# Kernel tuning notes

Measured on AMD Instinct MI355X. Metric: run time of the kernel, lower is better.

The kernel has to match this reference:

```python
import jax, jax.numpy as jnp
import numpy as np

B, N, C = 4, 2048, 768
H = 12
HD = C // H

def setup_inputs() -> dict:
    key = jax.random.key(0)
    k1, k2, k3, k4, k5 = jax.random.split(key, 5)
    x = jax.random.normal(k1, (B, N, C), dtype=jnp.float32)
    qkv_w = jax.random.normal(k2, (3 * C, C), dtype=jnp.float32) * (1.0 / np.sqrt(C))
    qkv_b = jax.random.normal(k3, (3 * C,), dtype=jnp.float32) * 0.02
    proj_w = jax.random.normal(k4, (C, C), dtype=jnp.float32) * (1.0 / np.sqrt(C))
    proj_b = jax.random.normal(k5, (C,), dtype=jnp.float32) * 0.02
    return {"x": x, "qkv_w": qkv_w, "qkv_b": qkv_b, "proj_w": proj_w, "proj_b": proj_b}

def reference(x, qkv_w, qkv_b, proj_w, proj_b):
    scale = HD ** (-0.5)
    # qkv projection: (B,N,3C)
    qkv = x @ qkv_w.T + qkv_b
    qkv = qkv.reshape(B, N, 3, H, HD).transpose(2, 0, 3, 1, 4)  # (3,B,H,N,HD)
    q, k, v = qkv[0], qkv[1], qkv[2]
    attn = jnp.einsum('bhqd,bhkd->bhqk', q, k) * scale  # (B,H,N,N)
    mask_value = -jnp.finfo(attn.dtype).max
    causal_mask = jnp.triu(jnp.ones((N, N), dtype=bool), k=1)
    attn = jnp.where(causal_mask, mask_value, attn)
    attn = jax.nn.softmax(attn, axis=-1)
    out = jnp.einsum('bhqk,bhkd->bhqd', attn, v)  # (B,H,N,HD)
    out = out.transpose(0, 2, 1, 3).reshape(B, N, C)
    return out @ proj_w.T + proj_b
```

## Files before the change

### kernel.cpp

```cpp
#include <hip/hip_runtime.h>
#include <hip/hip_bf16.h>


typedef __attribute__((ext_vector_type(8))) short bf16x8;
typedef __attribute__((ext_vector_type(4))) float f32x4;
typedef __attribute__((ext_vector_type(16))) float f32x16;

typedef __attribute__((address_space(3))) unsigned int lds_uint;
typedef __attribute__((address_space(1))) const unsigned int gbl_uint;

__device__ __forceinline__ void gload16(const void* g, void* l) {
  __builtin_amdgcn_global_load_lds((gbl_uint*)g, (lds_uint*)l, 16, 0, 0);
}

__device__ __forceinline__ unsigned short f2bf(float f) {
  unsigned u = __float_as_uint(f);
  unsigned rounding = 0x7FFFu + ((u >> 16) & 1u);
  return (unsigned short)((u + rounding) >> 16);
}

__device__ __forceinline__ unsigned cvtpk(float lo, float hi) {
  unsigned r;
  asm("v_cvt_pk_bf16_f32 %0, %1, %2" : "=v"(r) : "v"(lo), "v"(hi));
  return r;
}

__device__ __forceinline__ float exp2a(float x) {
  float r;
  asm("v_exp_f32 %0, %1" : "=v"(r) : "v"(x));
  return r;
}

__global__ void cast_f32_to_bf16(const float* __restrict__ in,
                                 unsigned short* __restrict__ out, int n) {
  int idx = blockIdx.x * blockDim.x + threadIdx.x;
  int stride = gridDim.x * blockDim.x;
  for (int i = idx * 4; i < n; i += stride * 4) {
    float4 v = *reinterpret_cast<const float4*>(in + i);
    ushort4 o;
    o.x = f2bf(v.x); o.y = f2bf(v.y); o.z = f2bf(v.z); o.w = f2bf(v.w);
    *reinterpret_cast<ushort4*>(out + i) = o;
  }
}

template <bool OUT_F32, int BN>
__global__ __launch_bounds__(256) void gemm_bt_kernel(
    const unsigned short* __restrict__ A,
    const unsigned short* __restrict__ Bw,
    const float* __restrict__ bias,
    void* __restrict__ Cout,
    int M, int Ncols, int K, int ldc, int nblk) {
  constexpr int NFRAG = BN / 32;
  __shared__ __align__(16) short As[2][4096];
  __shared__ __align__(16) short Bs[2][BN * 32];

  const int t = threadIdx.x;
  const int lane = t & 63;
  const int wave = t >> 6;
  const int wm = wave >> 1;
  const int wn = wave & 1;

  const int wid = blockIdx.x;
  const int xcd = wid & 7;
  const int idx = wid >> 3;
  const int m0 = (xcd * 8 + idx / nblk) * 128;
  const int n0 = (idx % nblk) * BN;

  const int lrow = lane & 15;
  const int lk = (lane >> 4) * 8;

  const int srow = t >> 2, scol = (t & 3) * 8;
  const unsigned short* gA0 = A + (size_t)(m0 + srow) * K + scol;
  const unsigned short* gA1 = gA0 + (size_t)64 * K;
  const unsigned short* gB0 = Bw + (size_t)(n0 + srow) * K + scol;
  const unsigned short* gB1 = gB0 + (size_t)64 * K;
  const int db0 = wave * 512, db1 = 2048 + wave * 512;

  f32x4 acc[4][NFRAG] = {};
  const int nk = K / 32;

  gload16(gA0, &As[0][db0]); gload16(gA1, &As[0][db1]);
  gload16(gB0, &Bs[0][db0]);
  if (BN == 128) gload16(gB1, &Bs[0][db1]);

  int cur = 0;
  for (int kk = 0; kk < nk; ++kk) {
    __syncthreads();
    if (kk + 1 < nk) {
      const int off = (kk + 1) * 32;
      gload16(gA0 + off, &As[cur ^ 1][db0]); gload16(gA1 + off, &As[cur ^ 1][db1]);
      gload16(gB0 + off, &Bs[cur ^ 1][db0]);
      if (BN == 128) gload16(gB1 + off, &Bs[cur ^ 1][db1]);
    }
    bf16x8 a[4], b[NFRAG];
#pragma unroll
    for (int m = 0; m < 4; ++m)
      a[m] = *reinterpret_cast<const bf16x8*>(&As[cur][(wm * 64 + m * 16 + lrow) * 32 + lk]);
#pragma unroll
    for (int n = 0; n < NFRAG; ++n)
      b[n] = *reinterpret_cast<const bf16x8*>(&Bs[cur][(wn * (BN / 2) + n * 16 + lrow) * 32 + lk]);
#pragma unroll
    for (int m = 0; m < 4; ++m)
#pragma unroll
      for (int n = 0; n < NFRAG; ++n)
        acc[m][n] = __builtin_amdgcn_mfma_f32_16x16x32_bf16(a[m], b[n], acc[m][n], 0, 0, 0);
    cur ^= 1;
  }

  const int orow0 = (lane >> 4) * 4;
  const int ocol = lane & 15;
#pragma unroll
  for (int m = 0; m < 4; ++m) {
#pragma unroll
    for (int n = 0; n < NFRAG; ++n) {
      const int c = n0 + wn * (BN / 2) + n * 16 + ocol;
      const float bv = bias[c];
#pragma unroll
      for (int r = 0; r < 4; ++r) {
        const int rr = m0 + wm * 64 + m * 16 + orow0 + r;
        const float v = acc[m][n][r] + bv;
        if (OUT_F32)
          reinterpret_cast<float*>(Cout)[(size_t)rr * ldc + c] = v;
        else
          reinterpret_cast<unsigned short*>(Cout)[(size_t)rr * ldc + c] = f2bf(v);
      }
    }
  }
}

#define ATT_N 2048
#define ATT_H 12
#define QKV_LD 2304

__global__ __launch_bounds__(256) void transpose_v(
    const unsigned short* __restrict__ qkv, unsigned short* __restrict__ vt) {
  __shared__ __align__(16) short L[128 * 72];
  const int kb = blockIdx.x;
  const int bh = blockIdx.y;
  const int t = threadIdx.x;
  const int b = bh / ATT_H, h = bh % ATT_H;
  const int d0 = (t & 7) * 8;
  const int kl0 = t >> 3;
  const unsigned short* src =
      qkv + (size_t)(b * ATT_N + kb * 128) * QKV_LD + 1536 + h * 64 + d0;
#pragma unroll
  for (int r = 0; r < 4; ++r) {
    const int kl = kl0 + r * 32;
    bf16x8 v = *reinterpret_cast<const bf16x8*>(src + (size_t)kl * QKV_LD);
    *reinterpret_cast<bf16x8*>(&L[kl * 72 + d0]) = v;
  }
  __syncthreads();
  const int d = t >> 2;
  const int c = t & 3;
  unsigned short* dst = vt + (size_t)bh * 64 * ATT_N + (size_t)d * ATT_N + kb * 128;
#pragma unroll
  for (int cc = 0; cc < 4; ++cc) {
    const int kc = cc * 32 + c * 8;
    union { unsigned short s[8]; bf16x8 v; } U;
#pragma unroll
    for (int j = 0; j < 8; ++j) U.s[j] = (unsigned short)L[(kc + j) * 72 + d];
    *reinterpret_cast<bf16x8*>(dst + kc) = U.v;
  }
}

__global__ __launch_bounds__(256) void attn_kernel(
    const unsigned short* __restrict__ qkv,
    const unsigned short* __restrict__ vt,
    unsigned short* __restrict__ out) {
  __shared__ __align__(16) short Ks[2][4096];
  __shared__ __align__(16) short Vs[2][4096];

  const int t = threadIdx.x;
  const int lane = t & 63;
  const int w = t >> 6;
  const int hi = lane >> 5;
  const int l31 = lane & 31;

  const int wid = blockIdx.x;
  const int qb = 15 - (wid / 48);
  const int bh = wid % 48;
  const int b = bh / ATT_H;
  const int h = bh % ATT_H;

  const size_t rowbase = (size_t)b * ATT_N;
  const unsigned short* qptr = qkv + rowbase * QKV_LD + h * 64;
  const unsigned short* kptr = qptr + 768;
  const unsigned short* vtptr = vt + (size_t)bh * 64 * ATT_N;

  const int q0w = qb * 128 + w * 32;
  const int qg = q0w + l31;
  const int nt = (qb + 1) * 2;

  bf16x8 qf[4];
#pragma unroll
  for (int dk = 0; dk < 4; ++dk)
    qf[dk] = *reinterpret_cast<const bf16x8*>(
        qptr + (size_t)(q0w + l31) * QKV_LD + dk * 16 + hi * 8);

  f32x16 O0 = {}, O1 = {};
  float lrun = 0.f;

  int kKr[2], kKc[2];
#pragma unroll
  for (int c = 0; c < 2; ++c) {
    const int i = t + c * 256;
    const int f = i >> 6, ls = i & 63;
    kKr[c] = (f >> 2) * 32 + (ls & 31);
    kKc[c] = (f & 3) * 2 + (ls >> 5);
  }
  const unsigned short* gK0 = kptr + (size_t)kKr[0] * QKV_LD + kKc[0] * 8;
  const unsigned short* gK1 = kptr + (size_t)kKr[1] * QKV_LD + kKc[1] * 8;
  const unsigned short* gV0 = vtptr + (size_t)kKr[0] * ATT_N + kKc[0] * 8;
  const unsigned short* gV1 = vtptr + (size_t)kKr[1] * ATT_N + kKc[1] * 8;
  const int db0 = w * 512, db1 = 2048 + w * 512;

  gload16(gK0, &Ks[0][db0]); gload16(gK1, &Ks[0][db1]);
  gload16(gV0, &Vs[0][db0]); gload16(gV1, &Vs[0][db1]);

  int cur = 0;
  for (int kt = 0; kt < nt; ++kt) {
    const int k0 = kt * 64;
    __syncthreads();
    if (kt + 1 < nt) {
      const size_t advk = (size_t)(k0 + 64) * QKV_LD;
      gload16(gK0 + advk, &Ks[cur ^ 1][db0]); gload16(gK1 + advk, &Ks[cur ^ 1][db1]);
      gload16(gV0 + (k0 + 64), &Vs[cur ^ 1][db0]);
      gload16(gV1 + (k0 + 64), &Vs[cur ^ 1][db1]);
    }

    if (k0 <= q0w + 31) {
      f32x16 S0 = {}, S1 = {};
      __builtin_amdgcn_s_setprio(1);
#pragma unroll
      for (int dk = 0; dk < 4; ++dk) {
        bf16x8 kf = *reinterpret_cast<const bf16x8*>(&Ks[cur][(dk * 64 + lane) * 8]);
        S0 = __builtin_amdgcn_mfma_f32_32x32x16_bf16(kf, qf[dk], S0, 0, 0, 0);
      }
#pragma unroll
      for (int dk = 0; dk < 4; ++dk) {
        bf16x8 kf = *reinterpret_cast<const bf16x8*>(&Ks[cur][((4 + dk) * 64 + lane) * 8]);
        S1 = __builtin_amdgcn_mfma_f32_32x32x16_bf16(kf, qf[dk], S1, 0, 0, 0);
      }
      __builtin_amdgcn_s_setprio(0);

      const float scale2 = 0.18033688f;
      float p0[16], p1[16];
      if (k0 + 63 <= q0w) {
#pragma unroll
        for (int r = 0; r < 16; ++r) {
          p0[r] = exp2a(S0[r] * scale2);
          p1[r] = exp2a(S1[r] * scale2);
        }
      } else {
#pragma unroll
        for (int r = 0; r < 16; ++r) {
          int row = (r & 3) + 8 * (r >> 2) + 4 * hi;
          float e0 = (k0 + row > qg) ? -1e30f : S0[r] * scale2;
          float e1 = (k0 + 32 + row > qg) ? -1e30f : S1[r] * scale2;
          p0[r] = exp2a(e0);
          p1[r] = exp2a(e1);
        }
      }

      float sa = 0.f, sb = 0.f;
#pragma unroll
      for (int r = 0; r < 16; r += 2) { sa += p0[r] + p1[r]; sb += p0[r + 1] + p1[r + 1]; }
      float rsum = sa + sb;
      rsum += __shfl_xor(rsum, 32);
      lrun += rsum;

      bf16x8 Ub[4];
#pragma unroll
      for (int s = 0; s < 2; ++s) {
        unsigned pu[4][2];
#pragma unroll
        for (int m = 0; m < 4; ++m)
#pragma unroll
          for (int c = 0; c < 2; ++c)
            pu[m][c] = s ? cvtpk(p1[4 * m + 2 * c], p1[4 * m + 2 * c + 1])
                         : cvtpk(p0[4 * m + 2 * c], p0[4 * m + 2 * c + 1]);
#pragma unroll
        for (int tt = 0; tt < 2; ++tt) {
          unsigned s0v = hi ? pu[2 * tt][0] : pu[2 * tt + 1][0];
          unsigned s1v = hi ? pu[2 * tt][1] : pu[2 * tt + 1][1];
          unsigned r0 = __shfl_xor(s0v, 32);
          unsigned r1 = __shfl_xor(s1v, 32);
          union { unsigned u[4]; bf16x8 v; } U;
          U.u[0] = hi ? r0 : pu[2 * tt][0];
          U.u[1] = hi ? r1 : pu[2 * tt][1];
          U.u[2] = hi ? pu[2 * tt + 1][0] : r0;
          U.u[3] = hi ? pu[2 * tt + 1][1] : r1;
          Ub[s * 2 + tt] = U.v;
        }
      }

      __builtin_amdgcn_s_setprio(1);
#pragma unroll
      for (int ks = 0; ks < 4; ++ks) {
        bf16x8 vf0 = *reinterpret_cast<const bf16x8*>(&Vs[cur][(ks * 64 + lane) * 8]);
        O0 = __builtin_amdgcn_mfma_f32_32x32x16_bf16(vf0, Ub[ks], O0, 0, 0, 0);
        bf16x8 vf1 = *reinterpret_cast<const bf16x8*>(&Vs[cur][((4 + ks) * 64 + lane) * 8]);
        O1 = __builtin_amdgcn_mfma_f32_32x32x16_bf16(vf1, Ub[ks], O1, 0, 0, 0);
      }
      __builtin_amdgcn_s_setprio(0);
    }
    cur ^= 1;
  }

  const float inv = 1.0f / lrun;
  unsigned short* orow = out + (rowbase + q0w + l31) * 768 + h * 64;
#pragma unroll
  for (int half = 0; half < 2; ++half) {
    const f32x16& O = half ? O1 : O0;
#pragma unroll
    for (int m = 0; m < 4; ++m) {
      uint2 o2;
      o2.x = cvtpk(O[4 * m + 0] * inv, O[4 * m + 1] * inv);
      o2.y = cvtpk(O[4 * m + 2] * inv, O[4 * m + 3] * inv);
      *reinterpret_cast<uint2*>(orow + half * 32 + 8 * m + 4 * hi) = o2;
    }
  }
}

extern "C" void kernel_launch(void* const* d_in, const int* in_sizes, int n_in,
                              void* d_out, int out_size, void* d_ws, size_t ws_size,
                              hipStream_t stream) {
  const float* x = (const float*)d_in[0];
  const float* qkv_w = (const float*)d_in[1];
  const float* qkv_b = (const float*)d_in[2];
  const float* proj_w = (const float*)d_in[3];
  const float* proj_b = (const float*)d_in[4];
  float* out = (float*)d_out;

  unsigned short* x_bf = (unsigned short*)d_ws;
  unsigned short* qw_bf = x_bf + (size_t)8192 * 768;
  unsigned short* pw_bf = qw_bf + (size_t)2304 * 768;
  unsigned short* qkv = pw_bf + (size_t)768 * 768;
  unsigned short* attno = qkv + (size_t)8192 * 2304;
  unsigned short* vtb = attno + (size_t)8192 * 768;

  cast_f32_to_bf16<<<dim3(1024), dim3(256), 0, stream>>>(x, x_bf, 8192 * 768);
  cast_f32_to_bf16<<<dim3(512), dim3(256), 0, stream>>>(qkv_w, qw_bf, 2304 * 768);
  cast_f32_to_bf16<<<dim3(256), dim3(256), 0, stream>>>(proj_w, pw_bf, 768 * 768);

  gemm_bt_kernel<false, 128><<<dim3(1152), dim3(256), 0, stream>>>(
      x_bf, qw_bf, qkv_b, qkv, 8192, 2304, 768, 2304, 18);
  transpose_v<<<dim3(16, 48), dim3(256), 0, stream>>>(qkv, vtb);
  attn_kernel<<<dim3(768), dim3(256), 0, stream>>>(qkv, vtb, attno);
  gemm_bt_kernel<true, 64><<<dim3(768), dim3(256), 0, stream>>>(
      attno, pw_bf, proj_b, out, 8192, 768, 768, 768, 12);
}
```

Baseline: 147.0 us.

## Split long causal attention query blocks across two KV halves with merge kernel

Query blocks 8–15, which have the longest causal KV ranges, are now each processed by two workgroups that each cover half of the KV tiles. The short query blocks (0–7) still run unsplit. A constant table sets the block order so the heavy pieces are scheduled first. The split halves write unnormalized bf16 partial outputs and row sums into the reused x_bf/qw_bf workspace, and a new merge kernel adds them and normalizes. The aim is better load balance across CUs, at the cost of an extra launch, extra global traffic and bf16 rounding of the partials.

Result: slower. 152.6 us (+3.8%).

```diff
diff --git a/kernel.cpp b/kernel.cpp
--- a/kernel.cpp
+++ b/kernel.cpp
@@ -163,10 +163,16 @@
   }
 }
 
+__constant__ int kAttnOrd[24] = {
+    61, 63, 28, 57, 59, 53, 55, 24, 49, 51, 45, 47,
+    20, 41, 43, 37, 39, 16, 33, 35, 12, 8, 4, 0};
+
 __global__ __launch_bounds__(256) void attn_kernel(
     const unsigned short* __restrict__ qkv,
     const unsigned short* __restrict__ vt,
-    unsigned short* __restrict__ out) {
+    unsigned short* __restrict__ out,
+    unsigned short* __restrict__ pO,
+    float* __restrict__ pL) {
   __shared__ __align__(16) short Ks[2][4096];
   __shared__ __align__(16) short Vs[2][4096];
 
@@ -177,10 +183,16 @@
   const int l31 = lane & 31;
 
   const int wid = blockIdx.x;
-  const int qb = 15 - (wid / 48);
+  const int code = kAttnOrd[wid / 48];
   const int bh = wid % 48;
+  const int split = code & 1;
+  const int hf = (code >> 1) & 1;
+  const int qb = code >> 2;
   const int b = bh / ATT_H;
   const int h = bh % ATT_H;
+
+  const int kt0 = split ? hf * (qb + 1) : 0;
+  const int kt1 = split ? (hf + 1) * (qb + 1) : 2 * (qb + 1);
 
   const size_t rowbase = (size_t)b * ATT_N;
   const unsigned short* qptr = qkv + rowbase * QKV_LD + h * 64;
@@ -189,7 +201,6 @@
 
   const int q0w = qb * 128 + w * 32;
   const int qg = q0w + l31;
-  const int nt = (qb + 1) * 2;
 
   bf16x8 qf[4];
 #pragma unroll
@@ -214,18 +225,21 @@
   const unsigned short* gV1 = vtptr + (size_t)kKr[1] * ATT_N + kKc[1] * 8;
   const int db0 = w * 512, db1 = 2048 + w * 512;
 
-  gload16(gK0, &Ks[0][db0]); gload16(gK1, &Ks[0][db1]);
-  gload16(gV0, &Vs[0][db0]); gload16(gV1, &Vs[0][db1]);
+  {
+    const size_t a0 = (size_t)kt0 * 64 * QKV_LD;
+    gload16(gK0 + a0, &Ks[0][db0]); gload16(gK1 + a0, &Ks[0][db1]);
+    gload16(gV0 + kt0 * 64, &Vs[0][db0]); gload16(gV1 + kt0 * 64, &Vs[0][db1]);
+  }
 
   int cur = 0;
-  for (int kt = 0; kt < nt; ++kt) {
+  for (int kt = kt0; kt < kt1; ++kt) {
     const int k0 = kt * 64;
     __syncthreads();
-    if (kt + 1 < nt) {
-      const size_t advk = (size_t)(k0 + 64) * QKV_LD;
+    if (kt + 1 < kt1) {
+      const size_t advk = (size_t)(kt + 1) * 64 * QKV_LD;
       gload16(gK0 + advk, &Ks[cur ^ 1][db0]); gload16(gK1 + advk, &Ks[cur ^ 1][db1]);
-      gload16(gV0 + (k0 + 64), &Vs[cur ^ 1][db0]);
-      gload16(gV1 + (k0 + 64), &Vs[cur ^ 1][db1]);
+      gload16(gV0 + (kt + 1) * 64, &Vs[cur ^ 1][db0]);
+      gload16(gV1 + (kt + 1) * 64, &Vs[cur ^ 1][db1]);
     }
 
     if (k0 <= q0w + 31) {
@@ -307,18 +321,63 @@
     cur ^= 1;
   }
 
-  const float inv = 1.0f / lrun;
-  unsigned short* orow = out + (rowbase + q0w + l31) * 768 + h * 64;
-#pragma unroll
-  for (int half = 0; half < 2; ++half) {
-    const f32x16& O = half ? O1 : O0;
-#pragma unroll
-    for (int m = 0; m < 4; ++m) {
-      uint2 o2;
-      o2.x = cvtpk(O[4 * m + 0] * inv, O[4 * m + 1] * inv);
-      o2.y = cvtpk(O[4 * m + 2] * inv, O[4 * m + 3] * inv);
-      *reinterpret_cast<uint2*>(orow + half * 32 + 8 * m + 4 * hi) = o2;
-    }
+  if (split) {
+    const size_t pidx = (((size_t)(qb - 8) * 2 + hf) * 48 + bh) * 128 + w * 32 + l31;
+    unsigned short* prow = pO + pidx * 64;
+#pragma unroll
+    for (int half = 0; half < 2; ++half) {
+      const f32x16& O = half ? O1 : O0;
+#pragma unroll
+      for (int m = 0; m < 4; ++m) {
+        uint2 o2;
+        o2.x = cvtpk(O[4 * m + 0], O[4 * m + 1]);
+        o2.y = cvtpk(O[4 * m + 2], O[4 * m + 3]);
+        *reinterpret_cast<uint2*>(prow + half * 32 + 8 * m + 4 * hi) = o2;
+      }
+    }
+    if (hi == 0) pL[pidx] = lrun;
+  } else {
+    const float inv = 1.0f / lrun;
+    unsigned short* orow = out + (rowbase + q0w + l31) * 768 + h * 64;
+#pragma unroll
+    for (int half = 0; half < 2; ++half) {
+      const f32x16& O = half ? O1 : O0;
+#pragma unroll
+      for (int m = 0; m < 4; ++m) {
+        uint2 o2;
+        o2.x = cvtpk(O[4 * m + 0] * inv, O[4 * m + 1] * inv);
+        o2.y = cvtpk(O[4 * m + 2] * inv, O[4 * m + 3] * inv);
+        *reinterpret_cast<uint2*>(orow + half * 32 + 8 * m + 4 * hi) = o2;
+      }
+    }
+  }
+}
+
+__global__ __launch_bounds__(256) void merge_attn(
+    const unsigned short* __restrict__ pO, const float* __restrict__ pL,
+    unsigned short* __restrict__ out) {
+  const int bid = blockIdx.x;
+  const int qh = bid / 48, bh = bid % 48;
+  const int b = bh / ATT_H, h = bh % ATT_H;
+  const int t = threadIdx.x;
+  const size_t base0 = ((size_t)(qh * 2 + 0) * 48 + bh) * 128;
+  const size_t base1 = ((size_t)(qh * 2 + 1) * 48 + bh) * 128;
+#pragma unroll
+  for (int i = 0; i < 4; ++i) {
+    const int c = t + i * 256;
+    const int row = c >> 3, d0 = (c & 7) * 8;
+    const float inv = 1.0f / (pL[base0 + row] + pL[base1 + row]);
+    bf16x8 a = *reinterpret_cast<const bf16x8*>(&pO[(base0 + row) * 64 + d0]);
+    bf16x8 bb = *reinterpret_cast<const bf16x8*>(&pO[(base1 + row) * 64 + d0]);
+    union { unsigned short s[8]; bf16x8 v; } U;
+#pragma unroll
+    for (int j = 0; j < 8; ++j) {
+      float fa = __uint_as_float(((unsigned)(unsigned short)a[j]) << 16);
+      float fb = __uint_as_float(((unsigned)(unsigned short)bb[j]) << 16);
+      U.s[j] = f2bf((fa + fb) * inv);
+    }
+    *reinterpret_cast<bf16x8*>(
+        &out[((size_t)b * ATT_N + (qh + 8) * 128 + row) * 768 + h * 64 + d0]) = U.v;
   }
 }
 
@@ -338,6 +397,8 @@
   unsigned short* qkv = pw_bf + (size_t)768 * 768;
   unsigned short* attno = qkv + (size_t)8192 * 2304;
   unsigned short* vtb = attno + (size_t)8192 * 768;
+  unsigned short* pO = x_bf;
+  float* pL = (float*)qw_bf;
 
   cast_f32_to_bf16<<<dim3(1024), dim3(256), 0, stream>>>(x, x_bf, 8192 * 768);
   cast_f32_to_bf16<<<dim3(512), dim3(256), 0, stream>>>(qkv_w, qw_bf, 2304 * 768);
@@ -346,7 +407,8 @@
   gemm_bt_kernel<false, 128><<<dim3(1152), dim3(256), 0, stream>>>(
       x_bf, qw_bf, qkv_b, qkv, 8192, 2304, 768, 2304, 18);
   transpose_v<<<dim3(16, 48), dim3(256), 0, stream>>>(qkv, vtb);
-  attn_kernel<<<dim3(768), dim3(256), 0, stream>>>(qkv, vtb, attno);
+  attn_kernel<<<dim3(1152), dim3(256), 0, stream>>>(qkv, vtb, attno, pO, pL);
+  merge_attn<<<dim3(384), dim3(256), 0, stream>>>(pO, pL, attno);
   gemm_bt_kernel<true, 64><<<dim3(768), dim3(256), 0, stream>>>(
       attno, pw_bf, proj_b, out, 8192, 768, 768, 768, 12);
 }
```
